# Performance work log

Measured on AMD Instinct MI355X. Metric: run time of the kernel, lower is better.

The kernel has to match this reference:

```python
import jax, jax.numpy as jnp
import numpy as np


def _filters():
    ident = jnp.array([[0., 0., 0.], [0., 1., 0.], [0., 0., 0.]], jnp.float32)
    sobel_x = jnp.array([[-1., 0., 1.], [-2., 0., 2.], [-1., 0., 1.]], jnp.float32)
    lap = jnp.array([[1., 2., 1.], [2., -12., 2.], [1., 2., 1.]], jnp.float32)
    return jnp.stack([ident, sobel_x, sobel_x.T, lap])  # [4,3,3]


def _perception(x):
    # depthwise conv with 4 fixed filters, circular padding; matches torch
    # reshape(b*ch,1,h,w) -> conv -> reshape(b, ch*4, h, w) channel ordering
    b, c, h, w = x.shape
    xp = jnp.pad(x, ((0, 0), (0, 0), (1, 1), (1, 1)), mode='wrap')
    y = xp.reshape(b * c, 1, h + 2, w + 2)
    k = _filters()[:, None]  # [4,1,3,3]
    y = jax.lax.conv_general_dilated(
        y, k, window_strides=(1, 1), padding='VALID',
        dimension_numbers=('NCHW', 'OIHW', 'NCHW'))  # [b*c,4,h,w]
    return y.reshape(b, c * 4, h, w)


def setup_inputs() -> dict:
    key = jax.random.key(0)
    k1, k2, k3, k4, k5 = jax.random.split(key, 5)
    B, C, H, W = 32, 12, 256, 256
    FC = 96
    xavier_std = 0.2 * np.sqrt(2.0 / (4 * C + FC))  # xavier_normal gain=0.2
    return {
        'x': jax.random.normal(k1, (B, C, H, W), jnp.float32),
        'w1': jax.random.normal(k2, (FC, 4 * C), jnp.float32) * xavier_std,
        'b1': jax.random.normal(k3, (FC,), jnp.float32) * 0.01,
        'w2': jax.random.normal(k4, (C, FC), jnp.float32) * 0.02,
        'rand_mask': jax.random.uniform(k5, (B, 1, H, W), jnp.float32),
    }


def reference(x, w1, b1, w2, rand_mask):
    update_rate = 0.5
    y = _perception(x)  # [B, 4C, H, W]
    hidden = jax.nn.relu(jnp.einsum('oc,bchw->bohw', w1, y) + b1[None, :, None, None])
    y = jnp.einsum('oc,bchw->bohw', w2, hidden)  # [B, C, H, W]
    update_mask = jnp.floor(rand_mask + update_rate)  # bernoulli(update_rate)
    return x + y * update_mask
```

## Files before the change

### kernel.cpp

```cpp
#include <hip/hip_runtime.h>
#include <stdint.h>

#define NC 12
#define NHW (256*256)
#define RSTR 136
#define CSTR 840

typedef __attribute__((ext_vector_type(8))) short bf16x8;
typedef __attribute__((ext_vector_type(4))) float f32x4;
typedef __attribute__((ext_vector_type(4))) uint32_t u32x4;
typedef __attribute__((ext_vector_type(2))) __bf16 bf16x2v;

__device__ __forceinline__ uint32_t pkbf(float lo, float hi) {
    bf16x2v v = { (__bf16)lo, (__bf16)hi };
    return __builtin_bit_cast(uint32_t, v);
}
#define PIN(v) asm volatile("" : "+v"(v))

__global__ __launch_bounds__(256, 4) void nca_fused9(
    const float* __restrict__ x, const float* __restrict__ w1,
    const float* __restrict__ b1, const float* __restrict__ w2,
    const float* __restrict__ rmask, float* __restrict__ out)
{
    __shared__ float smem[12 * CSTR];

    const int tid  = threadIdx.x;
    const int lane = tid & 63;
    const int wv   = tid >> 6;
    const int g    = lane >> 4;
    const int p    = lane & 15;
    const int c0   = 3 * g;

    u32x4 a1u[6][2];
    f32x4 biasv[6];
    #pragma unroll
    for (int t = 0; t < 6; ++t) {
        const int row = 16*t + p;
        const float4 fa = *reinterpret_cast<const float4*>(w1 + row*48 + 12*g + 0);
        const float4 fb = *reinterpret_cast<const float4*>(w1 + row*48 + 12*g + 4);
        const float4 fc = *reinterpret_cast<const float4*>(w1 + row*48 + 12*g + 8);
        a1u[t][0] = (u32x4){ pkbf(fa.x, fa.y), pkbf(fa.z, fa.w), pkbf(fb.x, fb.y), pkbf(fb.z, fb.w) };
        a1u[t][1] = (u32x4){ pkbf(fc.x, fc.y), pkbf(fc.z, fc.w), 0u, 0u };
        biasv[t] = *reinterpret_cast<const f32x4*>(b1 + 16*t + 4*g);
        PIN(a1u[t][0]); PIN(a1u[t][1]); PIN(biasv[t]);
    }
    u32x4 a2u[3];
    {
        const int rp = p & 3, gp = p >> 2;
        const int chA = 4*rp + ((gp + rp) & 3);
        #pragma unroll
        for (int s = 0; s < 3; ++s) {
            u32x4 u = {0u, 0u, 0u, 0u};
            if (rp < 3) {
                const float4 wa = *reinterpret_cast<const float4*>(w2 + chA*96 + 32*s + 4*g);
                const float4 wb = *reinterpret_cast<const float4*>(w2 + chA*96 + 32*s + 16 + 4*g);
                u = (u32x4){ pkbf(wa.x, wa.y), pkbf(wa.z, wa.w), pkbf(wb.x, wb.y), pkbf(wb.z, wb.w) };
            }
            a2u[s] = u;
            PIN(a2u[s]);
        }
    }

    const int b     = blockIdx.x >> 7;
    const int strip = (blockIdx.x >> 1) & 63;
    const int half  = blockIdx.x & 1;
    const int ra    = strip << 2;
    const int c0g   = half << 7;
    const float* __restrict__ xb = x + (size_t)b * NC * NHW;
    const float* __restrict__ mb = rmask + (size_t)b * NHW;
    float* __restrict__ ob = out + (size_t)b * NC * NHW;

    {
        const int q = tid >> 5;
        const int l = tid & 31;
        #pragma unroll
        for (int j = 0; j < 9; ++j) {
            const int hr  = 8*j + q;
            const int c   = hr / 6;
            const int r   = hr - 6*c;
            const int row = (ra + 255 + r) & 255;
            const f32x4 v = *reinterpret_cast<const f32x4*>(xb + c*NHW + (row << 8) + c0g + (l << 2));
            *reinterpret_cast<f32x4*>(&smem[c*CSTR + r*RSTR + 4 + (l << 2)]) = v;
        }
        if (tid < 144) {
            const int hr  = tid >> 1;
            const int side= tid & 1;
            const int c   = hr / 6;
            const int r   = hr - 6*c;
            const int row = (ra + 255 + r) & 255;
            const int col = side ? ((c0g + 128) & 255) : ((c0g + 255) & 255);
            smem[c*CSTR + r*RSTR + (side ? 132 : 3)] = xb[c*NHW + (row << 8) + col];
        }
    }
    __syncthreads();

    const int h    = ra + wv;
    const int hrow = h << 8;

    const float* tp[3][3];
    #pragma unroll
    for (int ci = 0; ci < 3; ++ci)
        #pragma unroll
        for (int q = 0; q < 3; ++q)
            tp[ci][q] = &smem[(c0 + ci)*CSTR + (wv + q)*RSTR + 3 + p];
    const float* xepi[3];
    float*       obp[3];
    #pragma unroll
    for (int r = 0; r < 3; ++r) {
        const int ch = 4*r + ((g + r) & 3);
        xepi[r] = &smem[ch*CSTR + (wv + 1)*RSTR + 4 + p];
        obp[r]  = ob + ch*NHW + hrow + c0g + p;
    }
    const float* mbp = mb + hrow + c0g + p;

    #pragma unroll
    for (int grp = 0; grp < 8; ++grp) {
        const int o = grp << 4;

        uint32_t yw[6];
        #pragma unroll
        for (int ci = 0; ci < 3; ++ci) {
            const float v0 = tp[ci][0][o+0], v1 = tp[ci][0][o+1], v2 = tp[ci][0][o+2];
            const float v3 = tp[ci][1][o+0], v4 = tp[ci][1][o+1], v5 = tp[ci][1][o+2];
            const float v6 = tp[ci][2][o+0], v7 = tp[ci][2][o+1], v8 = tp[ci][2][o+2];
            const float fsx = (v2 - v0) + 2.f*(v5 - v3) + (v8 - v6);
            const float fsy = (v6 - v0) + 2.f*(v7 - v1) + (v8 - v2);
            const float flp = ((v0 + v2) + (v6 + v8)) + 2.f*((v1 + v3) + (v5 + v7)) - 12.f*v4;
            yw[2*ci]   = pkbf(v4, fsx);
            yw[2*ci+1] = pkbf(fsy, flp);
        }
        const bf16x8 yf0 = __builtin_bit_cast(bf16x8, (u32x4){yw[0], yw[1], yw[2], yw[3]});
        const bf16x8 yf1 = __builtin_bit_cast(bf16x8, (u32x4){yw[4], yw[5], 0u, 0u});

        __builtin_amdgcn_s_setprio(1);
        uint32_t pu[6][2];
        #pragma unroll
        for (int t = 0; t < 6; ++t) {
            f32x4 acc = biasv[t];
            acc = __builtin_amdgcn_mfma_f32_16x16x32_bf16(__builtin_bit_cast(bf16x8, a1u[t][0]), yf0, acc, 0, 0, 0);
            acc = __builtin_amdgcn_mfma_f32_16x16x32_bf16(__builtin_bit_cast(bf16x8, a1u[t][1]), yf1, acc, 0, 0, 0);
            pu[t][0] = pkbf(fmaxf(acc[0], 0.f), fmaxf(acc[1], 0.f));
            pu[t][1] = pkbf(fmaxf(acc[2], 0.f), fmaxf(acc[3], 0.f));
        }
        f32x4 acc2 = {0.f, 0.f, 0.f, 0.f};
        #pragma unroll
        for (int s2 = 0; s2 < 3; ++s2) {
            const u32x4 fb2 = { pu[2*s2][0], pu[2*s2][1], pu[2*s2+1][0], pu[2*s2+1][1] };
            acc2 = __builtin_amdgcn_mfma_f32_16x16x32_bf16(__builtin_bit_cast(bf16x8, a2u[s2]), __builtin_bit_cast(bf16x8, fb2), acc2, 0, 0, 0);
        }
        __builtin_amdgcn_s_setprio(0);

        const float um = floorf(mbp[o] + 0.5f);
        #pragma unroll
        for (int r = 0; r < 3; ++r)
            obp[r][o] = xepi[r][o] + acc2[r] * um;
    }
}

extern "C" void kernel_launch(void* const* d_in, const int* in_sizes, int n_in,
                              void* d_out, int out_size, void* d_ws, size_t ws_size,
                              hipStream_t stream) {
    const float* x  = (const float*)d_in[0];
    const float* w1 = (const float*)d_in[1];
    const float* b1 = (const float*)d_in[2];
    const float* w2 = (const float*)d_in[3];
    const float* rm = (const float*)d_in[4];
    float* out = (float*)d_out;
    nca_fused9<<<dim3(32 * 64 * 2), dim3(256), 0, stream>>>(x, w1, b1, w2, rm, out);
}
```

Measured before the change: 86.29 us.

## Halve block tile width, remap output channels, use hardware bf16 pack

Each block now covers a 4-row by 64-column tile instead of 4x128, so the grid is twice as large and shared memory per block is roughly halved. That allows more resident blocks and better latency hiding, at the cost of more halo overhead. The w2 row mapping changes so each lane group writes channels 3g..3g+2, which lets the residual add reuse the centre stencil value already in registers instead of re-reading LDS. The activation pack uses the v_cvt_pk_bf16_f32 instruction and the stencil arithmetic is restructured into fewer ops with FMAs.

```diff
diff --git a/kernel.cpp b/kernel.cpp
--- a/kernel.cpp
+++ b/kernel.cpp
@@ -3,8 +3,8 @@
 
 #define NC 12
 #define NHW (256*256)
-#define RSTR 136
-#define CSTR 840
+#define RSTR 72
+#define CSTR 432
 
 typedef __attribute__((ext_vector_type(8))) short bf16x8;
 typedef __attribute__((ext_vector_type(4))) float f32x4;
@@ -12,12 +12,17 @@
 typedef __attribute__((ext_vector_type(2))) __bf16 bf16x2v;
 
 __device__ __forceinline__ uint32_t pkbf(float lo, float hi) {
+    uint32_t r;
+    asm("v_cvt_pk_bf16_f32 %0, %1, %2" : "=v"(r) : "v"(lo), "v"(hi));
+    return r;
+}
+__device__ __forceinline__ uint32_t pkbf_c(float lo, float hi) {
     bf16x2v v = { (__bf16)lo, (__bf16)hi };
     return __builtin_bit_cast(uint32_t, v);
 }
 #define PIN(v) asm volatile("" : "+v"(v))
 
-__global__ __launch_bounds__(256, 4) void nca_fused9(
+__global__ __launch_bounds__(256, 4) void nca_fused10(
     const float* __restrict__ x, const float* __restrict__ w1,
     const float* __restrict__ b1, const float* __restrict__ w2,
     const float* __restrict__ rmask, float* __restrict__ out)
@@ -39,57 +44,58 @@
         const float4 fa = *reinterpret_cast<const float4*>(w1 + row*48 + 12*g + 0);
         const float4 fb = *reinterpret_cast<const float4*>(w1 + row*48 + 12*g + 4);
         const float4 fc = *reinterpret_cast<const float4*>(w1 + row*48 + 12*g + 8);
-        a1u[t][0] = (u32x4){ pkbf(fa.x, fa.y), pkbf(fa.z, fa.w), pkbf(fb.x, fb.y), pkbf(fb.z, fb.w) };
-        a1u[t][1] = (u32x4){ pkbf(fc.x, fc.y), pkbf(fc.z, fc.w), 0u, 0u };
+        a1u[t][0] = (u32x4){ pkbf_c(fa.x, fa.y), pkbf_c(fa.z, fa.w), pkbf_c(fb.x, fb.y), pkbf_c(fb.z, fb.w) };
+        a1u[t][1] = (u32x4){ pkbf_c(fc.x, fc.y), pkbf_c(fc.z, fc.w), 0u, 0u };
         biasv[t] = *reinterpret_cast<const f32x4*>(b1 + 16*t + 4*g);
         PIN(a1u[t][0]); PIN(a1u[t][1]); PIN(biasv[t]);
     }
     u32x4 a2u[3];
     {
         const int rp = p & 3, gp = p >> 2;
-        const int chA = 4*rp + ((gp + rp) & 3);
+        const int chA = 3*gp + rp;
         #pragma unroll
         for (int s = 0; s < 3; ++s) {
             u32x4 u = {0u, 0u, 0u, 0u};
             if (rp < 3) {
                 const float4 wa = *reinterpret_cast<const float4*>(w2 + chA*96 + 32*s + 4*g);
                 const float4 wb = *reinterpret_cast<const float4*>(w2 + chA*96 + 32*s + 16 + 4*g);
-                u = (u32x4){ pkbf(wa.x, wa.y), pkbf(wa.z, wa.w), pkbf(wb.x, wb.y), pkbf(wb.z, wb.w) };
+                u = (u32x4){ pkbf_c(wa.x, wa.y), pkbf_c(wa.z, wa.w), pkbf_c(wb.x, wb.y), pkbf_c(wb.z, wb.w) };
             }
             a2u[s] = u;
             PIN(a2u[s]);
         }
     }
 
-    const int b     = blockIdx.x >> 7;
-    const int strip = (blockIdx.x >> 1) & 63;
-    const int half  = blockIdx.x & 1;
-    const int ra    = strip << 2;
-    const int c0g   = half << 7;
+    const int b    = blockIdx.x >> 8;
+    const int rem  = blockIdx.x & 255;
+    const int ra   = (rem >> 2) << 2;
+    const int c0q  = (rem & 3) << 6;
     const float* __restrict__ xb = x + (size_t)b * NC * NHW;
     const float* __restrict__ mb = rmask + (size_t)b * NHW;
     float* __restrict__ ob = out + (size_t)b * NC * NHW;
 
     {
-        const int q = tid >> 5;
-        const int l = tid & 31;
         #pragma unroll
-        for (int j = 0; j < 9; ++j) {
-            const int hr  = 8*j + q;
-            const int c   = hr / 6;
-            const int r   = hr - 6*c;
-            const int row = (ra + 255 + r) & 255;
-            const f32x4 v = *reinterpret_cast<const f32x4*>(xb + c*NHW + (row << 8) + c0g + (l << 2));
-            *reinterpret_cast<f32x4*>(&smem[c*CSTR + r*RSTR + 4 + (l << 2)]) = v;
+        for (int k = 0; k < 5; ++k) {
+            const int u = tid + (k << 8);
+            if (k < 4 || tid < 128) {
+                const int pair  = u >> 4;
+                const int chunk = u & 15;
+                const int c  = pair / 6;
+                const int r_ = pair - 6*c;
+                const int row = (ra + 255 + r_) & 255;
+                const f32x4 v = *reinterpret_cast<const f32x4*>(xb + c*NHW + (row << 8) + c0q + (chunk << 2));
+                *reinterpret_cast<f32x4*>(&smem[c*CSTR + r_*RSTR + 4 + (chunk << 2)]) = v;
+            }
         }
         if (tid < 144) {
             const int hr  = tid >> 1;
             const int side= tid & 1;
             const int c   = hr / 6;
-            const int r   = hr - 6*c;
-            const int row = (ra + 255 + r) & 255;
-            const int col = side ? ((c0g + 128) & 255) : ((c0g + 255) & 255);
-            smem[c*CSTR + r*RSTR + (side ? 132 : 3)] = xb[c*NHW + (row << 8) + col];
+            const int r_  = hr - 6*c;
+            const int row = (ra + 255 + r_) & 255;
+            const int col = side ? ((c0q + 64) & 255) : ((c0q + 255) & 255);
+            smem[c*CSTR + r_*RSTR + (side ? 68 : 3)] = xb[c*NHW + (row << 8) + col];
         }
     }
     __syncthreads();
@@ -97,37 +103,37 @@
     const int h    = ra + wv;
     const int hrow = h << 8;
 
-    const float* tp[3][3];
+    int tb[3];
     #pragma unroll
-    for (int ci = 0; ci < 3; ++ci)
-        #pragma unroll
-        for (int q = 0; q < 3; ++q)
-            tp[ci][q] = &smem[(c0 + ci)*CSTR + (wv + q)*RSTR + 3 + p];
-    const float* xepi[3];
-    float*       obp[3];
+    for (int ci = 0; ci < 3; ++ci) tb[ci] = (c0 + ci)*CSTR + wv*RSTR + 3 + p;
+    float* obp[3];
     #pragma unroll
-    for (int r = 0; r < 3; ++r) {
-        const int ch = 4*r + ((g + r) & 3);
-        xepi[r] = &smem[ch*CSTR + (wv + 1)*RSTR + 4 + p];
-        obp[r]  = ob + ch*NHW + hrow + c0g + p;
-    }
-    const float* mbp = mb + hrow + c0g + p;
+    for (int r = 0; r < 3; ++r) obp[r] = ob + (c0 + r)*NHW + hrow + c0q + p;
+    const float* mbp = mb + hrow + c0q + p;
 
     #pragma unroll
-    for (int grp = 0; grp < 8; ++grp) {
+    for (int grp = 0; grp < 4; ++grp) {
         const int o = grp << 4;
 
         uint32_t yw[6];
+        float xm[3];
         #pragma unroll
         for (int ci = 0; ci < 3; ++ci) {
-            const float v0 = tp[ci][0][o+0], v1 = tp[ci][0][o+1], v2 = tp[ci][0][o+2];
-            const float v3 = tp[ci][1][o+0], v4 = tp[ci][1][o+1], v5 = tp[ci][1][o+2];
-            const float v6 = tp[ci][2][o+0], v7 = tp[ci][2][o+1], v8 = tp[ci][2][o+2];
-            const float fsx = (v2 - v0) + 2.f*(v5 - v3) + (v8 - v6);
-            const float fsy = (v6 - v0) + 2.f*(v7 - v1) + (v8 - v2);
-            const float flp = ((v0 + v2) + (v6 + v8)) + 2.f*((v1 + v3) + (v5 + v7)) - 12.f*v4;
+            const int tbc = tb[ci] + o;
+            const float v0 = smem[tbc+0],        v1 = smem[tbc+1],        v2 = smem[tbc+2];
+            const float v3 = smem[tbc+RSTR],     v4 = smem[tbc+RSTR+1],   v5 = smem[tbc+RSTR+2];
+            const float v6 = smem[tbc+2*RSTR],   v7 = smem[tbc+2*RSTR+1], v8 = smem[tbc+2*RSTR+2];
+            const float s0 = v0 + v2, d0 = v2 - v0;
+            const float s1 = v3 + v5, d1 = v5 - v3;
+            const float s2 = v6 + v8, d2 = v8 - v6;
+            const float t0 = fmaf(2.f, v1, s0);
+            const float t2 = fmaf(2.f, v7, s2);
+            const float fsx = fmaf(2.f, d1, d0 + d2);
+            const float fsy = t2 - t0;
+            const float lap = fmaf(-12.f, v4, fmaf(2.f, s1, t0 + t2));
             yw[2*ci]   = pkbf(v4, fsx);
-            yw[2*ci+1] = pkbf(fsy, flp);
+            yw[2*ci+1] = pkbf(fsy, lap);
+            xm[ci] = v4;
         }
         const bf16x8 yf0 = __builtin_bit_cast(bf16x8, (u32x4){yw[0], yw[1], yw[2], yw[3]});
         const bf16x8 yf1 = __builtin_bit_cast(bf16x8, (u32x4){yw[4], yw[5], 0u, 0u});
@@ -153,7 +159,7 @@
         const float um = floorf(mbp[o] + 0.5f);
         #pragma unroll
         for (int r = 0; r < 3; ++r)
-            obp[r][o] = xepi[r][o] + acc2[r] * um;
+            obp[r][o] = xm[r] + acc2[r] * um;
     }
 }
 
@@ -166,5 +172,5 @@
     const float* w2 = (const float*)d_in[3];
     const float* rm = (const float*)d_in[4];
     float* out = (float*)d_out;
-    nca_fused9<<<dim3(32 * 64 * 2), dim3(256), 0, stream>>>(x, w1, b1, w2, rm, out);
+    nca_fused10<<<dim3(32 * 64 * 4), dim3(256), 0, stream>>>(x, w1, b1, w2, rm, out);
 }
```

After: 92.66 us. 1.07x slower.
